# Optimization experiments

Hardware: AMD Instinct MI355X
Metric: run time of the kernel (lower is better)

## Reference

```python
import jax, jax.numpy as jnp
import numpy as np

N_NODES = 50000
N_EDGES = 1600000
IN_DIM = 128
N_HEADS = 8
OUT_DIM = 16
LEAKY_SLOPE = 0.2


def setup_inputs() -> dict:
    key = jax.random.key(0)
    k1, k2, k3, k4, k5, k6 = jax.random.split(key, 6)
    x = jax.random.normal(k1, (N_NODES, IN_DIM), dtype=jnp.float32)
    W = jax.random.normal(k2, (N_HEADS * OUT_DIM, IN_DIM), dtype=jnp.float32) * (1.414 / np.sqrt(IN_DIM))
    attn_l = jax.random.normal(k3, (N_HEADS, OUT_DIM), dtype=jnp.float32) * 0.5
    attn_r = jax.random.normal(k4, (N_HEADS, OUT_DIM), dtype=jnp.float32) * 0.5
    src = jax.random.randint(k5, (N_EDGES,), 0, N_NODES, dtype=jnp.int64) if jax.config.jax_enable_x64 else jax.random.randint(k5, (N_EDGES,), 0, N_NODES, dtype=jnp.int32)
    dst = jax.random.randint(k6, (N_EDGES,), 0, N_NODES, dtype=src.dtype)
    return {"x": x, "W": W, "attn_l": attn_l, "attn_r": attn_r, "src": src, "dst": dst}


def reference(x, W, attn_l, attn_r, src, dst):
    n = x.shape[0]
    # fc projection -> [N, H, D]
    ft = (x @ W.T).reshape(n, N_HEADS, OUT_DIM)
    # per-node attention logits (bmm with [H,D,1] vector == contraction over D) -> [N, H]
    a1 = jnp.einsum('nhd,hd->nh', ft, attn_l)
    a2 = jnp.einsum('nhd,hd->nh', ft, attn_r)
    # per-edge score: leaky_relu(a1[src] + a2[dst]) -> [E, H]
    e = jax.nn.leaky_relu(a1[src] + a2[dst], negative_slope=LEAKY_SLOPE)
    # segment softmax over incoming edges of each dst node (numerically stable)
    seg_max = jax.ops.segment_max(e, dst, num_segments=n)          # [N, H]
    seg_max = jnp.where(jnp.isfinite(seg_max), seg_max, 0.0)       # isolated nodes -> 0
    e_exp = jnp.exp(e - seg_max[dst])                              # [E, H]
    denom = jax.ops.segment_sum(e_exp, dst, num_segments=n)        # [N, H]
    alpha = e_exp / denom[dst]                                     # [E, H]
    # weighted scatter-sum of src messages -> [N, H, D]
    msgs = ft[src] * alpha[:, :, None]                             # [E, H, D]
    out = jax.ops.segment_sum(msgs, dst, num_segments=n)
    return out
```

## Files before the change

### kernel.cpp

```cpp
#include <hip/hip_runtime.h>
#include <math.h>

#define N_NODES 50000
#define N_EDGES 1600000
#define IN_DIM 128
#define N_HEADS 8
#define OUT_DIM 16
#define HD 128
#define NBUCK 784
#define BCAP 2560
#define CHUNK 4096
#define BIN_BLOCKS ((N_EDGES + CHUNK - 1) / CHUNK)
#define NTILE 3125
#define PBLK ((NTILE + 3) / 4)
#define TROW 132
#define LOG2E 1.4426950408889634f

typedef __attribute__((ext_vector_type(8))) short bf16x8;
typedef __attribute__((ext_vector_type(4))) float f32x4;

__device__ __forceinline__ unsigned short f2bf(float f) {
    union { float f; unsigned int u; } v; v.f = f;
    unsigned int u = v.u;
    unsigned int r = (u + 0x7fffu + ((u >> 16) & 1u)) >> 16;
    return (unsigned short)r;
}

__device__ __forceinline__ void scan_nbuck_excl(int* arr, int* part) {
    int t = threadIdx.x;
    int v0 = 0, v1 = 0, v2 = 0, v3 = 0, cs = 0;
    if (t < NBUCK / 4) {
        v0 = arr[4 * t]; v1 = arr[4 * t + 1]; v2 = arr[4 * t + 2]; v3 = arr[4 * t + 3];
        cs = v0 + v1 + v2 + v3;
    }
    part[t] = cs;
    __syncthreads();
    for (int d = 1; d < 256; d <<= 1) {
        int u = (t >= d) ? part[t - d] : 0;
        __syncthreads();
        part[t] += u;
        __syncthreads();
    }
    if (t < NBUCK / 4) {
        int run = part[t] - cs;
        arr[4 * t] = run; run += v0;
        arr[4 * t + 1] = run; run += v1;
        arr[4 * t + 2] = run; run += v2;
        arr[4 * t + 3] = run;
    }
    __syncthreads();
}

__global__ void k_prep(const float* __restrict__ W, unsigned short* __restrict__ Wb,
                       int* __restrict__ bucket_cnt, int* __restrict__ ovf_cnt,
                       unsigned short* __restrict__ ftb, float* __restrict__ a1) {
    int g = blockIdx.x * 256 + threadIdx.x;
    if (g < NBUCK) bucket_cnt[g] = 0;
    if (g == 0) *ovf_cnt = 0;
    if (g < 64) ((unsigned int*)(ftb + (size_t)N_NODES * HD))[g] = 0u;
    if (g >= 64 && g < 64 + N_HEADS)
        a1[(size_t)N_NODES * N_HEADS + (g - 64)] = __int_as_float(0xff800000);
    if (g >= (HD * IN_DIM) / 4) return;
    float4 v = ((const float4*)W)[g];
    ushort4 us;
    us.x = f2bf(v.x); us.y = f2bf(v.y); us.z = f2bf(v.z); us.w = f2bf(v.w);
    ((ushort4*)Wb)[g] = us;
}

__global__ __launch_bounds__(256) void k_proj_bin(
    const float* __restrict__ x, const unsigned short* __restrict__ Wb,
    const float* __restrict__ attn_l, const float* __restrict__ attn_r,
    unsigned short* __restrict__ ftb, float* __restrict__ a1, float* __restrict__ a2,
    const int* __restrict__ src, const int* __restrict__ dst,
    unsigned int* __restrict__ region, int* __restrict__ bucket_cnt,
    int* __restrict__ ovf_cnt, unsigned int* __restrict__ ovf) {
    __shared__ __align__(16) char smem[4 * 16 * TROW * 4];
    int tid = threadIdx.x;

    if (blockIdx.x < PBLK) {
        int wid  = tid >> 6;
        int tile = blockIdx.x * 4 + wid;
        if (tile >= NTILE) return;
        int lane = tid & 63;
        int m = lane & 15, q = lane >> 4;
        int node0 = tile * 16;

        const float* xr = x + (size_t)(node0 + m) * IN_DIM + q * 8;
        float4 xa[4][2];
#pragma unroll
        for (int ks = 0; ks < 4; ks++) {
            xa[ks][0] = *(const float4*)(xr + ks * 32);
            xa[ks][1] = *(const float4*)(xr + ks * 32 + 4);
        }
        bf16x8 afr[4];
#pragma unroll
        for (int ks = 0; ks < 4; ks++) {
            afr[ks][0] = (short)f2bf(xa[ks][0].x); afr[ks][1] = (short)f2bf(xa[ks][0].y);
            afr[ks][2] = (short)f2bf(xa[ks][0].z); afr[ks][3] = (short)f2bf(xa[ks][0].w);
            afr[ks][4] = (short)f2bf(xa[ks][1].x); afr[ks][5] = (short)f2bf(xa[ks][1].y);
            afr[ks][6] = (short)f2bf(xa[ks][1].z); afr[ks][7] = (short)f2bf(xa[ks][1].w);
        }

        float* tl = (float*)smem + wid * (16 * TROW);

#pragma unroll
        for (int h = 0; h < N_HEADS; h++) {
            const unsigned short* wrow = Wb + (size_t)(h * 16 + m) * IN_DIM + q * 8;
            f32x4 c = {0.f, 0.f, 0.f, 0.f};
#pragma unroll
            for (int ks = 0; ks < 4; ks++) {
                bf16x8 bfr = *(const bf16x8*)(wrow + ks * 32);
                c = __builtin_amdgcn_mfma_f32_16x16x32_bf16(afr[ks], bfr, c, 0, 0, 0);
            }
#pragma unroll
            for (int r = 0; r < 4; r++)
                tl[(q * 4 + r) * TROW + h * 16 + m] = c[r];
        }

        int nd = lane & 15;
#pragma unroll
        for (int hi = 0; hi < 2; hi++) {
            int hh = (lane >> 4) + hi * 4;
            const float4* rowv = (const float4*)(tl + nd * TROW + hh * 16);
            const float4* alv  = (const float4*)(attn_l + hh * OUT_DIM);
            const float4* arv  = (const float4*)(attn_r + hh * OUT_DIM);
            float sl = 0.f, sr = 0.f;
#pragma unroll
            for (int d4 = 0; d4 < 4; d4++) {
                float4 fv = rowv[d4];
                float4 al = alv[d4];
                float4 ar = arv[d4];
                sl += fv.x * al.x + fv.y * al.y + fv.z * al.z + fv.w * al.w;
                sr += fv.x * ar.x + fv.y * ar.y + fv.z * ar.z + fv.w * ar.w;
            }
            a1[(node0 + nd) * N_HEADS + hh] = sl * LOG2E;
            a2[(node0 + nd) * N_HEADS + hh] = sr * LOG2E;
        }

#pragma unroll
        for (int p = 0; p < 4; p++) {
            int r = p * 4 + q;
            const float* srcp = tl + r * TROW + m * 8;
            float4 f0 = *(const float4*)(srcp);
            float4 f1 = *(const float4*)(srcp + 4);
            ushort4 u0, u1;
            u0.x = f2bf(f0.x); u0.y = f2bf(f0.y); u0.z = f2bf(f0.z); u0.w = f2bf(f0.w);
            u1.x = f2bf(f1.x); u1.y = f2bf(f1.y); u1.z = f2bf(f1.z); u1.w = f2bf(f1.w);
            ushort4* dstp = (ushort4*)(ftb + (size_t)(node0 + r) * HD + m * 8);
            dstp[0] = u0;
            dstp[1] = u1;
        }
    } else {
        unsigned int* stage = (unsigned int*)smem;
        int* hist  = (int*)(smem + 16384);
        int* delta = (int*)(smem + 19520);
        int* part  = (int*)(smem + 22656);

        int t = tid;
        int base = (blockIdx.x - PBLK) * CHUNK;
        int nvalid = min(CHUNK, N_EDGES - base);

        for (int i = t; i < NBUCK; i += 256) hist[i] = 0;
        __syncthreads();

        unsigned int mypack[CHUNK / 256];
#pragma unroll
        for (int k = 0; k < CHUNK / 256; k++) {
            int i = t + k * 256;
            if (i < nvalid) {
                int s = src[base + i];
                int d = dst[base + i];
                unsigned int p = ((unsigned int)d << 16) | (unsigned int)s;
                mypack[k] = p;
                atomicAdd(&hist[d >> 6], 1);
            }
        }
        __syncthreads();
        for (int i = t; i < NBUCK; i += 256) {
            int h = hist[i];
            delta[i] = (h > 0) ? atomicAdd(&bucket_cnt[i], h) : 0;
        }
        __syncthreads();
        scan_nbuck_excl(hist, part);
        for (int i = t; i < NBUCK; i += 256) delta[i] -= hist[i];
        __syncthreads();
#pragma unroll
        for (int k = 0; k < CHUNK / 256; k++) {
            int i = t + k * 256;
            if (i < nvalid) {
                unsigned int p = mypack[k];
                int slot = atomicAdd(&hist[p >> 22], 1);
                stage[slot] = p;
            }
        }
        __syncthreads();
        for (int i = t; i < nvalid; i += 256) {
            unsigned int p = stage[i];
            int b = p >> 22;
            int pos = delta[b] + i;
            if (pos < BCAP) region[(size_t)b * BCAP + pos] = p;
            else { int o = atomicAdd(ovf_cnt, 1); ovf[o] = p; }
        }
    }
}

__global__ __launch_bounds__(256) void k_place(
    const unsigned int* __restrict__ region, const int* __restrict__ bucket_cnt,
    const int* __restrict__ ovf_cnt, const unsigned int* __restrict__ ovf,
    int* __restrict__ offs, unsigned short* __restrict__ esrc) {
    int b = blockIdx.x;
    int t = threadIdx.x;
    __shared__ int sb[NBUCK], part[256];
    __shared__ int hist[64], sc[64], curs[64];
    __shared__ unsigned short sstage[BCAP];

    for (int i = t; i < NBUCK; i += 256) sb[i] = bucket_cnt[i];
    if (t < 64) hist[t] = 0;
    __syncthreads();
    scan_nbuck_excl(sb, part);

    int truec = bucket_cnt[b];
    int base_b = sb[b];
    int rc = min(truec, BCAP);
    bool fits = (truec <= BCAP);
    const unsigned int* reg = region + (size_t)b * BCAP;

    for (int i = t; i < rc; i += 256) atomicAdd(&hist[(reg[i] >> 16) & 63], 1);
    int no = 0;
    if (truec > BCAP) {
        no = *ovf_cnt;
        for (int i = t; i < no; i += 256)
            if ((int)(ovf[i] >> 22) == b) atomicAdd(&hist[(ovf[i] >> 16) & 63], 1);
    }
    __syncthreads();
    int h = (t < 64) ? hist[t] : 0;
    if (t < 64) sc[t] = h;
    __syncthreads();
    for (int d = 1; d < 64; d <<= 1) {
        int u = (t >= d && t < 64) ? sc[t - d] : 0;
        __syncthreads();
        if (t < 64) sc[t] += u;
        __syncthreads();
    }
    if (t < 64) {
        int pos0 = base_b + sc[t] - h;
        int node = b * 64 + t;
        if (node < N_NODES) offs[node] = pos0;
        curs[t] = pos0;
    }
    if (b == 0 && t == 0) offs[N_NODES] = N_EDGES;
    __syncthreads();
    for (int i = t; i < rc; i += 256) {
        unsigned int p = reg[i];
        int pos = atomicAdd(&curs[(p >> 16) & 63], 1);
        if (fits) sstage[pos - base_b] = (unsigned short)(p & 0xffffu);
        else      esrc[pos] = (unsigned short)(p & 0xffffu);
    }
    if (truec > BCAP) {
        for (int i = t; i < no; i += 256) {
            unsigned int p = ovf[i];
            if ((int)(p >> 22) == b) {
                int pos = atomicAdd(&curs[(p >> 16) & 63], 1);
                esrc[pos] = (unsigned short)(p & 0xffffu);
            }
        }
    }
    __syncthreads();
    if (fits) {
        for (int i = t; i < truec; i += 256)
            esrc[base_b + i] = sstage[i];
    }
}

__device__ __forceinline__ void consume16(const float* a1v, const unsigned int* p,
                                          float a2h, float& l, float& accx, float& accy) {
#pragma unroll
    for (int k = 0; k < 16; k++) {
        float t = a1v[k] + a2h;
        float u = fmaxf(t, 0.2f * t);
        float e;
        asm("v_exp_f32 %0, %1" : "=v"(e) : "v"(u));
        l += e;
        accx = fmaf(e, __uint_as_float(p[k] << 16), accx);
        accy = fmaf(e, __uint_as_float(p[k] & 0xffff0000u), accy);
    }
}

template <int GB>
__device__ __forceinline__ void issue16(int sv, const float* __restrict__ a1,
                                        const unsigned short* __restrict__ ftb,
                                        int hl, int dimoff,
                                        float* a1v, unsigned int* p) {
#pragma unroll
    for (int k = 0; k < 16; k++) {
        int s = __builtin_amdgcn_readlane(sv, GB + k);
        a1v[k] = a1[(size_t)s * N_HEADS + hl];
        p[k]   = *(const unsigned int*)(ftb + (size_t)s * HD + dimoff);
    }
}

__global__ __launch_bounds__(256, 4) void k_aggregate(
    const unsigned short* __restrict__ ftb, const float* __restrict__ a1,
    const float* __restrict__ a2, const int* __restrict__ offs,
    const unsigned short* __restrict__ esrc, float* __restrict__ out) {
    int wid  = threadIdx.x >> 6;
    int lane = threadIdx.x & 63;
    int node = blockIdx.x * 4 + wid;

    int off = __builtin_amdgcn_readfirstlane(offs[node]);
    int deg = __builtin_amdgcn_readfirstlane(offs[node + 1]) - off;
    int hl = lane >> 3;
    float a2h = a2[node * N_HEADS + hl];
    int dimoff = lane * 2;

    const unsigned short* ep = esrc + off;
    float accx = 0.f, accy = 0.f, l = 0.f;

    int done = 0;
    while (done < deg) {
        int nb = deg - done;
        if (nb > 64) nb = 64;
        int v = (int)ep[done + lane];
        int sv = (lane < nb) ? v : N_NODES;

        float a1A[16], a1B[16];
        unsigned int pA[16], pB[16];
        issue16<0>(sv, a1, ftb, hl, dimoff, a1A, pA);
        if (nb > 16) issue16<16>(sv, a1, ftb, hl, dimoff, a1B, pB);
        consume16(a1A, pA, a2h, l, accx, accy);
        if (nb > 32) issue16<32>(sv, a1, ftb, hl, dimoff, a1A, pA);
        if (nb > 16) consume16(a1B, pB, a2h, l, accx, accy);
        if (nb > 48) issue16<48>(sv, a1, ftb, hl, dimoff, a1B, pB);
        if (nb > 32) consume16(a1A, pA, a2h, l, accx, accy);
        if (nb > 48) consume16(a1B, pB, a2h, l, accx, accy);
        done += 64;
    }

    float invl = (deg > 0) ? 1.f / l : 0.f;
    float2 o; o.x = accx * invl; o.y = accy * invl;
    *(float2*)(out + (size_t)node * HD + dimoff) = o;
}

extern "C" void kernel_launch(void* const* d_in, const int* in_sizes, int n_in,
                              void* d_out, int out_size, void* d_ws, size_t ws_size,
                              hipStream_t stream) {
    const float* x      = (const float*)d_in[0];
    const float* W      = (const float*)d_in[1];
    const float* attn_l = (const float*)d_in[2];
    const float* attn_r = (const float*)d_in[3];
    const int*   src    = (const int*)d_in[4];
    const int*   dst    = (const int*)d_in[5];
    float* out = (float*)d_out;

    char* ws = (char*)d_ws;
    size_t o = 0;
    auto alloc = [&](size_t bytes) -> char* {
        char* p = ws + o;
        o = (o + bytes + 255) & ~(size_t)255;
        return p;
    };
    unsigned short* ftb  = (unsigned short*)alloc((size_t)(N_NODES + 1) * HD * 2);
    float* a1            = (float*)alloc((size_t)(N_NODES + 1) * N_HEADS * 4);
    float* a2            = (float*)alloc((size_t)N_NODES * N_HEADS * 4);
    unsigned short* Wb   = (unsigned short*)alloc((size_t)HD * IN_DIM * 2);
    unsigned int* region = (unsigned int*)alloc((size_t)NBUCK * BCAP * 4);
    int* bucket_cnt      = (int*)alloc((size_t)NBUCK * 4);
    int* ovf_cnt         = (int*)alloc(4);
    unsigned int* ovf    = (unsigned int*)alloc((size_t)N_EDGES * 4);
    int* offs            = (int*)alloc((size_t)(N_NODES + 1) * 4);
    unsigned short* esrc = (unsigned short*)alloc((size_t)N_EDGES * 2 + 256);

    (void)in_sizes; (void)n_in; (void)out_size; (void)ws_size;

    k_prep<<<16, 256, 0, stream>>>(W, Wb, bucket_cnt, ovf_cnt, ftb, a1);
    k_proj_bin<<<PBLK + BIN_BLOCKS, 256, 0, stream>>>(
        x, Wb, attn_l, attn_r, ftb, a1, a2,
        src, dst, region, bucket_cnt, ovf_cnt, ovf);
    k_place<<<NBUCK, 256, 0, stream>>>(region, bucket_cnt, ovf_cnt, ovf, offs, esrc);
    k_aggregate<<<N_NODES / 4, 256, 0, stream>>>(ftb, a1, a2, offs, esrc, out);
}
```

Baseline: 195.1 us.

## Fuse CSR placement into aggregation using per-bucket shared-memory edge lists

Merges the placement kernel and the aggregation kernel into one. Each block sorts its bucket's edges by destination in shared memory, then its four waves each aggregate 16 nodes straight from that local list. This removes the global offs/esrc arrays, the global prefix scan and one launch. In exchange there are only 784 blocks instead of 12500, so the grid is smaller and per-wave work is serialized and more uneven. Overflow edges are handled by a linear scan of the overflow list for every node.

```diff
diff --git a/kernel.cpp b/kernel.cpp
--- a/kernel.cpp
+++ b/kernel.cpp
@@ -204,74 +204,6 @@
     }
 }
 
-__global__ __launch_bounds__(256) void k_place(
-    const unsigned int* __restrict__ region, const int* __restrict__ bucket_cnt,
-    const int* __restrict__ ovf_cnt, const unsigned int* __restrict__ ovf,
-    int* __restrict__ offs, unsigned short* __restrict__ esrc) {
-    int b = blockIdx.x;
-    int t = threadIdx.x;
-    __shared__ int sb[NBUCK], part[256];
-    __shared__ int hist[64], sc[64], curs[64];
-    __shared__ unsigned short sstage[BCAP];
-
-    for (int i = t; i < NBUCK; i += 256) sb[i] = bucket_cnt[i];
-    if (t < 64) hist[t] = 0;
-    __syncthreads();
-    scan_nbuck_excl(sb, part);
-
-    int truec = bucket_cnt[b];
-    int base_b = sb[b];
-    int rc = min(truec, BCAP);
-    bool fits = (truec <= BCAP);
-    const unsigned int* reg = region + (size_t)b * BCAP;
-
-    for (int i = t; i < rc; i += 256) atomicAdd(&hist[(reg[i] >> 16) & 63], 1);
-    int no = 0;
-    if (truec > BCAP) {
-        no = *ovf_cnt;
-        for (int i = t; i < no; i += 256)
-            if ((int)(ovf[i] >> 22) == b) atomicAdd(&hist[(ovf[i] >> 16) & 63], 1);
-    }
-    __syncthreads();
-    int h = (t < 64) ? hist[t] : 0;
-    if (t < 64) sc[t] = h;
-    __syncthreads();
-    for (int d = 1; d < 64; d <<= 1) {
-        int u = (t >= d && t < 64) ? sc[t - d] : 0;
-        __syncthreads();
-        if (t < 64) sc[t] += u;
-        __syncthreads();
-    }
-    if (t < 64) {
-        int pos0 = base_b + sc[t] - h;
-        int node = b * 64 + t;
-        if (node < N_NODES) offs[node] = pos0;
-        curs[t] = pos0;
-    }
-    if (b == 0 && t == 0) offs[N_NODES] = N_EDGES;
-    __syncthreads();
-    for (int i = t; i < rc; i += 256) {
-        unsigned int p = reg[i];
-        int pos = atomicAdd(&curs[(p >> 16) & 63], 1);
-        if (fits) sstage[pos - base_b] = (unsigned short)(p & 0xffffu);
-        else      esrc[pos] = (unsigned short)(p & 0xffffu);
-    }
-    if (truec > BCAP) {
-        for (int i = t; i < no; i += 256) {
-            unsigned int p = ovf[i];
-            if ((int)(p >> 22) == b) {
-                int pos = atomicAdd(&curs[(p >> 16) & 63], 1);
-                esrc[pos] = (unsigned short)(p & 0xffffu);
-            }
-        }
-    }
-    __syncthreads();
-    if (fits) {
-        for (int i = t; i < truec; i += 256)
-            esrc[base_b + i] = sstage[i];
-    }
-}
-
 __device__ __forceinline__ void consume16(const float* a1v, const unsigned int* p,
                                           float a2h, float& l, float& accx, float& accy) {
 #pragma unroll
@@ -299,46 +231,98 @@
     }
 }
 
-__global__ __launch_bounds__(256, 4) void k_aggregate(
+__global__ __launch_bounds__(256, 4) void k_place_agg(
     const unsigned short* __restrict__ ftb, const float* __restrict__ a1,
-    const float* __restrict__ a2, const int* __restrict__ offs,
-    const unsigned short* __restrict__ esrc, float* __restrict__ out) {
-    int wid  = threadIdx.x >> 6;
-    int lane = threadIdx.x & 63;
-    int node = blockIdx.x * 4 + wid;
-
-    int off = __builtin_amdgcn_readfirstlane(offs[node]);
-    int deg = __builtin_amdgcn_readfirstlane(offs[node + 1]) - off;
+    const float* __restrict__ a2, const unsigned int* __restrict__ region,
+    const int* __restrict__ bucket_cnt, const int* __restrict__ ovf_cnt,
+    const unsigned int* __restrict__ ovf, float* __restrict__ out) {
+    int b = blockIdx.x;
+    int t = threadIdx.x;
+
+    __shared__ int hist[64], sc[64], curs[64], loff[65];
+    __shared__ unsigned short sstage[BCAP + 64];
+
+    int truec = bucket_cnt[b];
+    int rc = min(truec, BCAP);
+    const unsigned int* reg = region + (size_t)b * BCAP;
+
+    if (t < 64) hist[t] = 0;
+    __syncthreads();
+    for (int i = t; i < rc; i += 256) atomicAdd(&hist[(reg[i] >> 16) & 63], 1);
+    __syncthreads();
+    int h = (t < 64) ? hist[t] : 0;
+    if (t < 64) sc[t] = h;
+    __syncthreads();
+    for (int d = 1; d < 64; d <<= 1) {
+        int u = (t >= d && t < 64) ? sc[t - d] : 0;
+        __syncthreads();
+        if (t < 64) sc[t] += u;
+        __syncthreads();
+    }
+    if (t < 64) { loff[t] = sc[t] - h; curs[t] = sc[t] - h; }
+    if (t == 63) loff[64] = sc[63];
+    __syncthreads();
+    for (int i = t; i < rc; i += 256) {
+        unsigned int p = reg[i];
+        int pos = atomicAdd(&curs[(p >> 16) & 63], 1);
+        sstage[pos] = (unsigned short)(p & 0xffffu);
+    }
+    __syncthreads();
+
+    int wid  = t >> 6;
+    int lane = t & 63;
     int hl = lane >> 3;
-    float a2h = a2[node * N_HEADS + hl];
     int dimoff = lane * 2;
-
-    const unsigned short* ep = esrc + off;
-    float accx = 0.f, accy = 0.f, l = 0.f;
-
-    int done = 0;
-    while (done < deg) {
-        int nb = deg - done;
-        if (nb > 64) nb = 64;
-        int v = (int)ep[done + lane];
-        int sv = (lane < nb) ? v : N_NODES;
-
-        float a1A[16], a1B[16];
-        unsigned int pA[16], pB[16];
-        issue16<0>(sv, a1, ftb, hl, dimoff, a1A, pA);
-        if (nb > 16) issue16<16>(sv, a1, ftb, hl, dimoff, a1B, pB);
-        consume16(a1A, pA, a2h, l, accx, accy);
-        if (nb > 32) issue16<32>(sv, a1, ftb, hl, dimoff, a1A, pA);
-        if (nb > 16) consume16(a1B, pB, a2h, l, accx, accy);
-        if (nb > 48) issue16<48>(sv, a1, ftb, hl, dimoff, a1B, pB);
-        if (nb > 32) consume16(a1A, pA, a2h, l, accx, accy);
-        if (nb > 48) consume16(a1B, pB, a2h, l, accx, accy);
-        done += 64;
-    }
-
-    float invl = (deg > 0) ? 1.f / l : 0.f;
-    float2 o; o.x = accx * invl; o.y = accy * invl;
-    *(float2*)(out + (size_t)node * HD + dimoff) = o;
+    int no = __builtin_amdgcn_readfirstlane(*ovf_cnt);
+
+    for (int ni = 0; ni < 16; ni++) {
+        int nl = wid * 16 + ni;
+        int node = b * 64 + nl;
+        if (node >= N_NODES) break;
+        int st = __builtin_amdgcn_readfirstlane(loff[nl]);
+        int en = __builtin_amdgcn_readfirstlane(loff[nl + 1]);
+        float a2h = a2[(size_t)node * N_HEADS + hl];
+        float accx = 0.f, accy = 0.f, l = 0.f;
+
+        for (int done = st; done < en; done += 64) {
+            int nbc = en - done; if (nbc > 64) nbc = 64;
+            int v = (int)sstage[done + lane];
+            int sv = (lane < nbc) ? v : N_NODES;
+
+            float a1A[16], a1B[16];
+            unsigned int pA[16], pB[16];
+            issue16<0>(sv, a1, ftb, hl, dimoff, a1A, pA);
+            if (nbc > 16) issue16<16>(sv, a1, ftb, hl, dimoff, a1B, pB);
+            consume16(a1A, pA, a2h, l, accx, accy);
+            if (nbc > 32) issue16<32>(sv, a1, ftb, hl, dimoff, a1A, pA);
+            if (nbc > 16) consume16(a1B, pB, a2h, l, accx, accy);
+            if (nbc > 48) issue16<48>(sv, a1, ftb, hl, dimoff, a1B, pB);
+            if (nbc > 32) consume16(a1A, pA, a2h, l, accx, accy);
+            if (nbc > 48) consume16(a1B, pB, a2h, l, accx, accy);
+        }
+
+        if (no > 0) {
+            for (int i = 0; i < no; i++) {
+                unsigned int pk = ovf[i];
+                if ((int)(pk >> 16) == node) {
+                    int s = (int)(pk & 0xffffu);
+                    float a1v = a1[(size_t)s * N_HEADS + hl];
+                    unsigned int p = *(const unsigned int*)(ftb + (size_t)s * HD + dimoff);
+                    float tt = a1v + a2h;
+                    float uu = fmaxf(tt, 0.2f * tt);
+                    float ee;
+                    asm("v_exp_f32 %0, %1" : "=v"(ee) : "v"(uu));
+                    l += ee;
+                    accx = fmaf(ee, __uint_as_float(p << 16), accx);
+                    accy = fmaf(ee, __uint_as_float(p & 0xffff0000u), accy);
+                }
+            }
+        }
+
+        float invl = (l > 0.f) ? 1.f / l : 0.f;
+        float2 o; o.x = accx * invl; o.y = accy * invl;
+        *(float2*)(out + (size_t)node * HD + dimoff) = o;
+    }
 }
 
 extern "C" void kernel_launch(void* const* d_in, const int* in_sizes, int n_in,
@@ -367,8 +351,6 @@
     int* bucket_cnt      = (int*)alloc((size_t)NBUCK * 4);
     int* ovf_cnt         = (int*)alloc(4);
     unsigned int* ovf    = (unsigned int*)alloc((size_t)N_EDGES * 4);
-    int* offs            = (int*)alloc((size_t)(N_NODES + 1) * 4);
-    unsigned short* esrc = (unsigned short*)alloc((size_t)N_EDGES * 2 + 256);
 
     (void)in_sizes; (void)n_in; (void)out_size; (void)ws_size;
 
@@ -376,6 +358,6 @@
     k_proj_bin<<<PBLK + BIN_BLOCKS, 256, 0, stream>>>(
         x, Wb, attn_l, attn_r, ftb, a1, a2,
         src, dst, region, bucket_cnt, ovf_cnt, ovf);
-    k_place<<<NBUCK, 256, 0, stream>>>(region, bucket_cnt, ovf_cnt, ovf, offs, esrc);
-    k_aggregate<<<N_NODES / 4, 256, 0, stream>>>(ftb, a1, a2, offs, esrc, out);
-}
+    k_place_agg<<<NBUCK, 256, 0, stream>>>(ftb, a1, a2, region, bucket_cnt,
+                                           ovf_cnt, ovf, out);
+}
```

New measurement: 211.6 us. +8.5%, slower.
